# Optimization experiments

Hardware: AMD Instinct MI355X
Metric: run time of the kernel (lower is better)

## Reference

```python
import jax, jax.numpy as jnp
import numpy as np

B, T, D, H = 4, 2048, 1024, 16
HD = D // H


def setup_inputs() -> dict:
    key = jax.random.key(0)
    kq, kk, kv, k1, k2, k3, k4 = jax.random.split(key, 7)
    q = jax.random.normal(kq, (B, T, D), dtype=jnp.float32)
    k = jax.random.normal(kk, (B, T, D), dtype=jnp.float32)
    v = jax.random.normal(kv, (B, T, D), dtype=jnp.float32)
    # causal mask, broadcast over heads: [B, 1, T, T]
    mask = jnp.broadcast_to(jnp.tril(jnp.ones((T, T), dtype=bool)), (B, 1, T, T))
    s = 0.02
    Wq = jax.random.normal(k1, (D, D), dtype=jnp.float32) * s
    Wk = jax.random.normal(k2, (D, D), dtype=jnp.float32) * s
    Wv = jax.random.normal(k3, (D, D), dtype=jnp.float32) * s
    Wo = jax.random.normal(k4, (D, D), dtype=jnp.float32) * s
    return {"q": q, "k": k, "v": v, "mask": mask,
            "Wq": Wq, "Wk": Wk, "Wv": Wv, "Wo": Wo}


def reference(q, k, v, mask, Wq, Wk, Wv, Wo):
    scale = HD ** -0.5
    # nn.Linear: y = x @ W.T  (bias=False)
    qh = (q @ Wq.T).reshape(B, T, H, HD).transpose(0, 2, 1, 3)  # [B,H,T,HD]
    kh = (k @ Wk.T).reshape(B, -1, H, HD).transpose(0, 2, 1, 3)
    vh = (v @ Wv.T).reshape(B, -1, H, HD).transpose(0, 2, 1, 3)
    scores = jnp.einsum('bhqd,bhkd->bhqk', qh, kh) * scale  # [B,H,T,T]
    # dropout p=0.0 -> identity (applied pre-mask in original)
    scores = jnp.where(mask, scores, -jnp.inf)
    probs = jax.nn.softmax(scores, axis=-1)
    attn = jnp.einsum('bhqk,bhkd->bhqd', probs, vh)  # [B,H,T,HD]
    attn = attn.transpose(0, 2, 1, 3).reshape(B, T, D)
    return attn @ Wo.T
```

## Files before the change

kernel.cpp:

```cpp
#include <hip/hip_runtime.h>
#include <stdint.h>

#define B_  4
#define T_  2048
#define D_  1024
#define H_  16
#define HD_ 64
#define KK_ 1024

typedef __bf16 bf16_t;
typedef __bf16 bf16x8 __attribute__((ext_vector_type(8)));
typedef float  f32x4  __attribute__((ext_vector_type(4)));
typedef float  f32x16 __attribute__((ext_vector_type(16)));

__device__ __forceinline__ uint16_t f2bf(float f) {
  uint32_t x = __float_as_uint(f);
  uint32_t r = (x + 0x7fffu + ((x >> 16) & 1u)) >> 16;
  return (uint16_t)r;
}

__device__ __forceinline__ uint32_t pack2(float a, float b) {
  return (uint32_t)f2bf(a) | ((uint32_t)f2bf(b) << 16);
}

__device__ __forceinline__ float exp2a(float x) {
  float r;
  asm("v_exp_f32 %0, %1" : "=v"(r) : "v"(x));
  return r;
}

__device__ __forceinline__ uint32_t cvtpk(float a, float b) {
  uint32_t r;
  asm("v_cvt_pk_bf16_f32 %0, %1, %2" : "=v"(r) : "v"(a), "v"(b));
  return r;
}

__device__ __forceinline__ void plswap(uint32_t& a, uint32_t& b) {
  asm("v_permlane32_swap_b32 %0, %1" : "+v"(a), "+v"(b));
}

__device__ __forceinline__ void gll16(const void* g, void* l) {
  __builtin_amdgcn_global_load_lds(
      (const __attribute__((address_space(1))) void*)g,
      (__attribute__((address_space(3))) void*)l, 16, 0, 0);
}

__global__ __launch_bounds__(256) void cvt3(const float* __restrict__ s0,
                                            const float* __restrict__ s1,
                                            const float* __restrict__ s2,
                                            uint16_t* __restrict__ d0,
                                            uint16_t* __restrict__ d1,
                                            uint16_t* __restrict__ d2) {
  const float* in = blockIdx.y == 0 ? s0 : (blockIdx.y == 1 ? s1 : s2);
  uint16_t* out = blockIdx.y == 0 ? d0 : (blockIdx.y == 1 ? d1 : d2);
  int i = (blockIdx.x * 256 + threadIdx.x) * 8;
  float4 a = *(const float4*)(in + i);
  float4 b = *(const float4*)(in + i + 4);
  uint4 u;
  u.x = pack2(a.x, a.y);
  u.y = pack2(a.z, a.w);
  u.z = pack2(b.x, b.y);
  u.w = pack2(b.z, b.w);
  *(uint4*)(out + i) = u;
}

__global__ __launch_bounds__(256) void cvtW(const float* __restrict__ s0,
                                            const float* __restrict__ s1,
                                            const float* __restrict__ s2,
                                            const float* __restrict__ s3,
                                            uint16_t* __restrict__ d0,
                                            uint16_t* __restrict__ d1,
                                            uint16_t* __restrict__ d2,
                                            uint16_t* __restrict__ d3) {
  const float* in = blockIdx.y == 0 ? s0 : (blockIdx.y == 1 ? s1 :
                    (blockIdx.y == 2 ? s2 : s3));
  uint16_t* out = blockIdx.y == 0 ? d0 : (blockIdx.y == 1 ? d1 :
                  (blockIdx.y == 2 ? d2 : d3));
  int i = (blockIdx.x * 256 + threadIdx.x) * 8;
  float4 a = *(const float4*)(in + i);
  float4 b = *(const float4*)(in + i + 4);
  uint4 u;
  u.x = pack2(a.x, a.y);
  u.y = pack2(a.z, a.w);
  u.z = pack2(b.x, b.y);
  u.w = pack2(b.z, b.w);
  *(uint4*)(out + i) = u;
}

__global__ __launch_bounds__(512, 2)
void gemm8(const uint16_t* __restrict__ a0, const uint16_t* __restrict__ a1,
           const uint16_t* __restrict__ a2, const uint16_t* __restrict__ w0,
           const uint16_t* __restrict__ w1, const uint16_t* __restrict__ w2,
           void* __restrict__ o0, void* __restrict__ o1, void* __restrict__ o2,
           int mode_base, float scale0) {
  __shared__ __align__(16) uint16_t Ab[4][128 * 32];
  __shared__ __align__(16) uint16_t Bb[4][256 * 32];

  const int nwg = gridDim.x;
  const int bid = blockIdx.x;
  const int cpx = nwg >> 3;
  const int swz = (bid & 7) * cpx + (bid >> 3);
  const int g = swz >> 8;
  const int r = swz & 255;
  const int mt = r >> 2, nt = r & 3;
  const int m0 = mt * 128, n0 = nt * 256;

  const uint16_t* A = g == 0 ? a0 : (g == 1 ? a1 : a2);
  const uint16_t* W = g == 0 ? w0 : (g == 1 ? w1 : w2);
  void* Out = g == 0 ? o0 : (g == 1 ? o1 : o2);
  const int mode = mode_base + g;
  const float scale = (mode == 0) ? scale0 : 1.0f;

  const int tid = threadIdx.x;
  const int wid = tid >> 6, lane = tid & 63;
  const int fr = lane & 15, fq = lane >> 4;
  const int wm = wid >> 2, wn = wid & 3;

  f32x4 acc[4][4];
#pragma unroll
  for (int i = 0; i < 4; ++i)
#pragma unroll
    for (int j = 0; j < 4; ++j) acc[i][j] = (f32x4){0.f, 0.f, 0.f, 0.f};

  const int NT = KK_ / 32;

#define STAGE(bi, t)                                                          \
  do {                                                                        \
    {                                                                         \
      int row = wid * 16 + (lane >> 2);                                       \
      int ch = (lane & 3) ^ ((row >> 1) & 3);                                 \
      gll16(A + (size_t)(m0 + row) * KK_ + (t) * 32 + ch * 8,                 \
            &Ab[bi][wid * 512]);                                              \
    }                                                                         \
    _Pragma("unroll")                                                         \
    for (int c = 0; c < 2; ++c) {                                             \
      int row = c * 128 + wid * 16 + (lane >> 2);                             \
      int ch = (lane & 3) ^ ((row >> 1) & 3);                                 \
      gll16(W + (size_t)(n0 + row) * KK_ + (t) * 32 + ch * 8,                 \
            &Bb[bi][c * 4096 + wid * 512]);                                   \
    }                                                                         \
  } while (0)

  STAGE(0, 0);
  STAGE(1, 1);
  STAGE(2, 2);
  asm volatile("s_waitcnt vmcnt(6)" ::: "memory");
  __builtin_amdgcn_s_barrier();

#pragma unroll 4
  for (int t = 0; t < NT; ++t) {
    const int cur = t & 3;
    bf16x8 af[4], bfr[4];
#pragma unroll
    for (int i = 0; i < 4; ++i) {
      int ra = wm * 64 + i * 16 + fr;
      af[i] = *(const bf16x8*)&Ab[cur][ra * 32 + ((fq ^ ((ra >> 1) & 3)) << 3)];
      int rb = wn * 64 + i * 16 + fr;
      bfr[i] = *(const bf16x8*)&Bb[cur][rb * 32 + ((fq ^ ((rb >> 1) & 3)) << 3)];
    }
    if (t + 3 < NT) STAGE((t + 3) & 3, t + 3);
    __builtin_amdgcn_s_setprio(1);
#pragma unroll
    for (int mf = 0; mf < 4; ++mf)
#pragma unroll
      for (int nf = 0; nf < 4; ++nf)
        acc[mf][nf] = __builtin_amdgcn_mfma_f32_16x16x32_bf16(af[mf], bfr[nf],
                                                              acc[mf][nf], 0, 0, 0);
    __builtin_amdgcn_s_setprio(0);
    if (t + 1 < NT) {
      if (t + 3 < NT) {
        asm volatile("s_waitcnt vmcnt(6)" ::: "memory");
      } else if (t + 2 < NT) {
        asm volatile("s_waitcnt vmcnt(3)" ::: "memory");
      } else {
        asm volatile("s_waitcnt vmcnt(0)" ::: "memory");
      }
      __builtin_amdgcn_s_barrier();
    }
  }
#undef STAGE

#pragma unroll
  for (int mf = 0; mf < 4; ++mf) {
#pragma unroll
    for (int nf = 0; nf < 4; ++nf) {
      int m = m0 + wm * 64 + mf * 16 + fq * 4;
      int n = n0 + wn * 64 + nf * 16 + fr;
      if (mode == 2) {
        int b = m >> 11, t = m & (T_ - 1);
        int h = n >> 6, hd = n & 63;
        uint2 pk;
        pk.x = pack2(acc[mf][nf][0], acc[mf][nf][1]);
        pk.y = pack2(acc[mf][nf][2], acc[mf][nf][3]);
        uint16_t* dst = (uint16_t*)Out + ((((size_t)b * H_ + h) * HD_ + hd) * T_ + t);
        *(uint2*)dst = pk;
      } else if (mode == 3) {
#pragma unroll
        for (int rr = 0; rr < 4; ++rr)
          ((float*)Out)[(size_t)(m + rr) * D_ + n] = acc[mf][nf][rr];
      } else {
#pragma unroll
        for (int rr = 0; rr < 4; ++rr) {
          int mm = m + rr;
          int b = mm >> 11, t = mm & (T_ - 1);
          int h = n >> 6, hd = n & 63;
          ((uint16_t*)Out)[((((size_t)b * H_ + h) * T_ + t) << 6) + hd] =
              f2bf(acc[mf][nf][rr] * scale);
        }
      }
    }
  }
}

__global__ __launch_bounds__(512)
void attn_fwd(const uint16_t* __restrict__ Qh, const uint16_t* __restrict__ Kh,
              const uint16_t* __restrict__ Vt, uint16_t* __restrict__ O) {
  __shared__ __align__(16) uint16_t SB[4][64 * 64];

  const int tid = threadIdx.x, wid = tid >> 6, lane = tid & 63;
  const int ql = lane & 31, hi = lane >> 5;
  const int bid = blockIdx.x;
  const int qb = (T_ / 256 - 1) - (bid >> 6);
  const int bh = bid & 63;
  const int q0 = qb * 256;
  const int wq0 = q0 + wid * 32;
  const size_t hoff = (size_t)bh * T_ * HD_;
  const uint16_t* Qp = Qh + hoff;
  const uint16_t* Kp = Kh + hoff;
  const uint16_t* Vp = Vt + hoff;

  bf16x8 qf[4];
  {
    const uint16_t* qrow = Qp + (size_t)(wq0 + ql) * 64 + hi * 8;
#pragma unroll
    for (int ks = 0; ks < 4; ++ks) qf[ks] = *(const bf16x8*)(qrow + ks * 16);
  }

  float m = -1e30f, l = 0.f;
  f32x16 acc[2];
#pragma unroll
  for (int mo = 0; mo < 2; ++mo)
#pragma unroll
    for (int r = 0; r < 16; ++r) acc[mo][r] = 0.f;

  const int ntiles = 4 * qb + 4;

#define STAGE(buf, t)                                                        \
  do {                                                                       \
    int row = wid * 8 + (lane >> 3);                                         \
    int sw = ((lane & 7) ^ (row & 7)) << 3;                                  \
    gll16(Kp + (size_t)((t) * 64 + row) * 64 + sw, &SB[buf][wid * 512]);     \
    gll16(Vp + (size_t)row * T_ + (t) * 64 + sw, &SB[2 + (buf)][wid * 512]); \
  } while (0)

  STAGE(0, 0);
  asm volatile("s_waitcnt vmcnt(0)" ::: "memory");
  __builtin_amdgcn_s_barrier();

  for (int it = 0; it < ntiles; ++it) {
    const int cur = it & 1;
    if (it + 1 < ntiles) STAGE(cur ^ 1, it + 1);

    if (it * 64 <= wq0 + 31) {
      f32x16 st[2];
#pragma unroll
      for (int mm = 0; mm < 2; ++mm)
#pragma unroll
        for (int r = 0; r < 16; ++r) st[mm][r] = 0.f;
#pragma unroll
      for (int ks = 0; ks < 4; ++ks) {
#pragma unroll
        for (int mm = 0; mm < 2; ++mm) {
          int row = mm * 32 + ql;
          int ch = (ks * 2 + hi) ^ (row & 7);
          bf16x8 kf = *(const bf16x8*)&SB[cur][row * 64 + ch * 8];
          st[mm] = __builtin_amdgcn_mfma_f32_32x32x16_bf16(kf, qf[ks], st[mm], 0, 0, 0);
        }
      }

      if (it * 64 + 63 > wq0) {
        int qg = wq0 + ql;
#pragma unroll
        for (int mm = 0; mm < 2; ++mm)
#pragma unroll
          for (int r = 0; r < 16; ++r) {
            int kv = it * 64 + mm * 32 + (r & 3) + 8 * (r >> 2) + 4 * hi;
            if (kv > qg) st[mm][r] = -1e30f;
          }
      }

      float pm = st[0][0];
#pragma unroll
      for (int r = 1; r < 16; ++r) pm = fmaxf(pm, st[0][r]);
#pragma unroll
      for (int r = 0; r < 16; ++r) pm = fmaxf(pm, st[1][r]);
      pm = fmaxf(pm, __shfl_xor(pm, 32));

      if (__any(pm > m + 8.f)) {
        float mn = fmaxf(m, pm);
        float sf = exp2a(m - mn);
        m = mn;
        l *= sf;
#pragma unroll
        for (int mo = 0; mo < 2; ++mo)
#pragma unroll
          for (int r = 0; r < 16; ++r) acc[mo][r] *= sf;
      }

      float rs = 0.f;
#pragma unroll
      for (int mm = 0; mm < 2; ++mm)
#pragma unroll
        for (int r = 0; r < 16; ++r) {
          float p = exp2a(st[mm][r] - m);
          st[mm][r] = p;
          rs += p;
        }
      rs += __shfl_xor(rs, 32);
      l += rs;

      bf16x8 pf[4];
#pragma unroll
      for (int mm = 0; mm < 2; ++mm)
#pragma unroll
        for (int g = 0; g < 2; ++g) {
          uint32_t a1 = cvtpk(st[mm][8 * g + 0], st[mm][8 * g + 1]);
          uint32_t a2 = cvtpk(st[mm][8 * g + 2], st[mm][8 * g + 3]);
          uint32_t b1 = cvtpk(st[mm][8 * g + 4], st[mm][8 * g + 5]);
          uint32_t b2 = cvtpk(st[mm][8 * g + 6], st[mm][8 * g + 7]);
          plswap(a1, b1);
          plswap(a2, b2);
          union { uint32_t w[4]; bf16x8 v; } u;
          u.w[0] = a1; u.w[1] = a2; u.w[2] = b1; u.w[3] = b2;
          pf[mm * 2 + g] = u.v;
        }

#pragma unroll
      for (int ks = 0; ks < 4; ++ks) {
#pragma unroll
        for (int mo = 0; mo < 2; ++mo) {
          int row = mo * 32 + ql;
          int ch = (ks * 2 + hi) ^ (row & 7);
          bf16x8 vf = *(const bf16x8*)&SB[2 + cur][row * 64 + ch * 8];
          acc[mo] = __builtin_amdgcn_mfma_f32_32x32x16_bf16(vf, pf[ks], acc[mo], 0, 0, 0);
        }
      }
    }

    asm volatile("s_waitcnt vmcnt(0)" ::: "memory");
    __builtin_amdgcn_s_barrier();
  }
#undef STAGE

  __syncthreads();
  uint16_t* ost = &SB[0][0];
  {
    float inv = 1.0f / l;
    uint16_t* wst = ost + wid * 2048;
#pragma unroll
    for (int mo = 0; mo < 2; ++mo)
#pragma unroll
      for (int r = 0; r < 16; r += 2) {
        int hd = mo * 32 + (r & 3) + 8 * (r >> 2) + 4 * hi;
        uint32_t pk = pack2(acc[mo][r] * inv, acc[mo][r + 1] * inv);
        int col = hd ^ ((ql & 7) << 3);
        *(uint32_t*)&wst[ql * 64 + col] = pk;
      }
  }
  __syncthreads();
  {
    int row = tid >> 1, half = tid & 1;
    int r7 = row & 7;
    int b = bh >> 4, h = bh & 15;
    size_t g = (size_t)(b * T_ + q0 + row) * D_ + h * 64 + half * 32;
#pragma unroll
    for (int j = 0; j < 4; ++j) {
      int cc = half * 4 + j;
      uint4 val = *(const uint4*)&ost[row * 64 + (cc ^ r7) * 8];
      *(uint4*)&O[g + j * 8] = val;
    }
  }
}

extern "C" void kernel_launch(void* const* d_in, const int* in_sizes, int n_in,
                              void* d_out, int out_size, void* d_ws, size_t ws_size,
                              hipStream_t stream) {
  (void)in_sizes; (void)n_in; (void)out_size; (void)ws_size;
  const float* q  = (const float*)d_in[0];
  const float* k  = (const float*)d_in[1];
  const float* v  = (const float*)d_in[2];
  const float* Wq = (const float*)d_in[4];
  const float* Wk = (const float*)d_in[5];
  const float* Wv = (const float*)d_in[6];
  const float* Wo = (const float*)d_in[7];

  uint8_t* ws = (uint8_t*)d_ws;
  const size_t MB = 1u << 20;
  uint16_t* WQB = (uint16_t*)(ws + 0 * MB);
  uint16_t* WKB = (uint16_t*)(ws + 2 * MB);
  uint16_t* WVB = (uint16_t*)(ws + 4 * MB);
  uint16_t* WOB = (uint16_t*)(ws + 6 * MB);
  uint16_t* XQ  = (uint16_t*)(ws + 8 * MB);
  uint16_t* XK  = (uint16_t*)(ws + 24 * MB);
  uint16_t* XV  = (uint16_t*)(ws + 40 * MB);
  uint16_t* QH  = (uint16_t*)(ws + 56 * MB);
  uint16_t* KH  = (uint16_t*)(ws + 72 * MB);
  uint16_t* VT  = (uint16_t*)(ws + 88 * MB);
  uint16_t* AC  = (uint16_t*)(ws + 8 * MB);

  cvt3<<<dim3(B_ * T_ * D_ / 2048, 3), 256, 0, stream>>>(q, k, v, XQ, XK, XV);
  cvtW<<<dim3(D_ * D_ / 2048, 4), 256, 0, stream>>>(Wq, Wk, Wv, Wo, WQB, WKB, WVB, WOB);

  const float qscale = 0.125f * 1.44269504088896340736f;

  gemm8<<<dim3(768), 512, 0, stream>>>(XQ, XK, XV, WQB, WKB, WVB,
                                       QH, KH, VT, 0, qscale);

  attn_fwd<<<dim3(T_ / 256 * 64), 512, 0, stream>>>(QH, KH, VT, AC);

  gemm8<<<dim3(256), 512, 0, stream>>>(AC, nullptr, nullptr, WOB, nullptr, nullptr,
                                       d_out, nullptr, nullptr, 3, 1.0f);
}
```

Measured before the change: 175.7 us.

## Deepen GEMM K-tile to 64 and triple-buffer attention K/V loads

The projection GEMM moves from a 4-stage ring of 32-wide K tiles to a 3-stage ring of 64-wide K tiles. This halves the number of barrier and wait iterations and doubles the MFMA work between syncs, with a new XOR swizzle for the 64-wide rows. The attention kernel moves from double to triple buffering of K/V tiles, prefetching two tiles ahead and waiting with vmcnt(2) instead of draining all loads every iteration. Both changes use more LDS, which may lower occupancy.

```diff
diff --git a/kernel.cpp b/kernel.cpp
--- a/kernel.cpp
+++ b/kernel.cpp
@@ -93,8 +93,8 @@
            const uint16_t* __restrict__ w1, const uint16_t* __restrict__ w2,
            void* __restrict__ o0, void* __restrict__ o1, void* __restrict__ o2,
            int mode_base, float scale0) {
-  __shared__ __align__(16) uint16_t Ab[4][128 * 32];
-  __shared__ __align__(16) uint16_t Bb[4][256 * 32];
+  __shared__ __align__(16) uint16_t Ab[3][128 * 64];
+  __shared__ __align__(16) uint16_t Bb[3][256 * 64];
 
   const int nwg = gridDim.x;
   const int bid = blockIdx.x;
@@ -115,6 +115,7 @@
   const int wid = tid >> 6, lane = tid & 63;
   const int fr = lane & 15, fq = lane >> 4;
   const int wm = wid >> 2, wn = wid & 3;
+  const int srow = lane >> 3, c8 = lane & 7;
 
   f32x4 acc[4][4];
 #pragma unroll
@@ -122,61 +123,78 @@
 #pragma unroll
     for (int j = 0; j < 4; ++j) acc[i][j] = (f32x4){0.f, 0.f, 0.f, 0.f};
 
-  const int NT = KK_ / 32;
+  const int NT = KK_ / 64;
 
 #define STAGE(bi, t)                                                          \
   do {                                                                        \
-    {                                                                         \
-      int row = wid * 16 + (lane >> 2);                                       \
-      int ch = (lane & 3) ^ ((row >> 1) & 3);                                 \
-      gll16(A + (size_t)(m0 + row) * KK_ + (t) * 32 + ch * 8,                 \
-            &Ab[bi][wid * 512]);                                              \
+    _Pragma("unroll")                                                         \
+    for (int c = 0; c < 2; ++c) {                                             \
+      int row = c * 64 + wid * 8 + srow;                                      \
+      int sw = (c8 ^ (row & 7)) << 3;                                         \
+      gll16(A + (size_t)(m0 + row) * KK_ + (t) * 64 + sw,                     \
+            &Ab[bi][c * 4096 + wid * 512]);                                   \
     }                                                                         \
     _Pragma("unroll")                                                         \
-    for (int c = 0; c < 2; ++c) {                                             \
-      int row = c * 128 + wid * 16 + (lane >> 2);                             \
-      int ch = (lane & 3) ^ ((row >> 1) & 3);                                 \
-      gll16(W + (size_t)(n0 + row) * KK_ + (t) * 32 + ch * 8,                 \
+    for (int c = 0; c < 4; ++c) {                                             \
+      int row = c * 64 + wid * 8 + srow;                                      \
+      int sw = (c8 ^ (row & 7)) << 3;                                         \
+      gll16(W + (size_t)(n0 + row) * KK_ + (t) * 64 + sw,                     \
             &Bb[bi][c * 4096 + wid * 512]);                                   \
     }                                                                         \
   } while (0)
 
   STAGE(0, 0);
   STAGE(1, 1);
-  STAGE(2, 2);
   asm volatile("s_waitcnt vmcnt(6)" ::: "memory");
   __builtin_amdgcn_s_barrier();
 
-#pragma unroll 4
+  int cur = 0;
   for (int t = 0; t < NT; ++t) {
-    const int cur = t & 3;
-    bf16x8 af[4], bfr[4];
+    const uint16_t* Ac = &Ab[cur][0];
+    const uint16_t* Bc = &Bb[cur][0];
+    bf16x8 af0[4], bf0[4];
 #pragma unroll
     for (int i = 0; i < 4; ++i) {
       int ra = wm * 64 + i * 16 + fr;
-      af[i] = *(const bf16x8*)&Ab[cur][ra * 32 + ((fq ^ ((ra >> 1) & 3)) << 3)];
+      af0[i] = *(const bf16x8*)&Ac[ra * 64 + ((fq ^ (ra & 7)) << 3)];
       int rb = wn * 64 + i * 16 + fr;
-      bfr[i] = *(const bf16x8*)&Bb[cur][rb * 32 + ((fq ^ ((rb >> 1) & 3)) << 3)];
-    }
-    if (t + 3 < NT) STAGE((t + 3) & 3, t + 3);
+      bf0[i] = *(const bf16x8*)&Bc[rb * 64 + ((fq ^ (rb & 7)) << 3)];
+    }
+    if (t + 2 < NT) {
+      int nb = cur + 2; if (nb >= 3) nb -= 3;
+      STAGE(nb, t + 2);
+    }
+    bf16x8 af1[4], bf1[4];
+#pragma unroll
+    for (int i = 0; i < 4; ++i) {
+      int ra = wm * 64 + i * 16 + fr;
+      af1[i] = *(const bf16x8*)&Ac[ra * 64 + (((4 + fq) ^ (ra & 7)) << 3)];
+      int rb = wn * 64 + i * 16 + fr;
+      bf1[i] = *(const bf16x8*)&Bc[rb * 64 + (((4 + fq) ^ (rb & 7)) << 3)];
+    }
     __builtin_amdgcn_s_setprio(1);
 #pragma unroll
     for (int mf = 0; mf < 4; ++mf)
 #pragma unroll
       for (int nf = 0; nf < 4; ++nf)
-        acc[mf][nf] = __builtin_amdgcn_mfma_f32_16x16x32_bf16(af[mf], bfr[nf],
+        acc[mf][nf] = __builtin_amdgcn_mfma_f32_16x16x32_bf16(af0[mf], bf0[nf],
+                                                              acc[mf][nf], 0, 0, 0);
+#pragma unroll
+    for (int mf = 0; mf < 4; ++mf)
+#pragma unroll
+      for (int nf = 0; nf < 4; ++nf)
+        acc[mf][nf] = __builtin_amdgcn_mfma_f32_16x16x32_bf16(af1[mf], bf1[nf],
                                                               acc[mf][nf], 0, 0, 0);
     __builtin_amdgcn_s_setprio(0);
     if (t + 1 < NT) {
-      if (t + 3 < NT) {
+      if (t + 2 < NT) {
         asm volatile("s_waitcnt vmcnt(6)" ::: "memory");
-      } else if (t + 2 < NT) {
-        asm volatile("s_waitcnt vmcnt(3)" ::: "memory");
       } else {
         asm volatile("s_waitcnt vmcnt(0)" ::: "memory");
       }
       __builtin_amdgcn_s_barrier();
     }
+    ++cur; if (cur == 3) cur = 0;
   }
 #undef STAGE
 
@@ -215,7 +233,7 @@
 __global__ __launch_bounds__(512)
 void attn_fwd(const uint16_t* __restrict__ Qh, const uint16_t* __restrict__ Kh,
               const uint16_t* __restrict__ Vt, uint16_t* __restrict__ O) {
-  __shared__ __align__(16) uint16_t SB[4][64 * 64];
+  __shared__ __align__(16) uint16_t SB[6][64 * 64];
 
   const int tid = threadIdx.x, wid = tid >> 6, lane = tid & 63;
   const int ql = lane & 31, hi = lane >> 5;
@@ -250,16 +268,20 @@
     int row = wid * 8 + (lane >> 3);                                         \
     int sw = ((lane & 7) ^ (row & 7)) << 3;                                  \
     gll16(Kp + (size_t)((t) * 64 + row) * 64 + sw, &SB[buf][wid * 512]);     \
-    gll16(Vp + (size_t)row * T_ + (t) * 64 + sw, &SB[2 + (buf)][wid * 512]); \
+    gll16(Vp + (size_t)row * T_ + (t) * 64 + sw, &SB[3 + (buf)][wid * 512]); \
   } while (0)
 
   STAGE(0, 0);
-  asm volatile("s_waitcnt vmcnt(0)" ::: "memory");
+  if (ntiles > 1) STAGE(1, 1);
+  asm volatile("s_waitcnt vmcnt(2)" ::: "memory");
   __builtin_amdgcn_s_barrier();
 
+  int cur = 0;
   for (int it = 0; it < ntiles; ++it) {
-    const int cur = it & 1;
-    if (it + 1 < ntiles) STAGE(cur ^ 1, it + 1);
+    if (it + 2 < ntiles) {
+      int nb = cur + 2; if (nb >= 3) nb -= 3;
+      STAGE(nb, it + 2);
+    }
 
     if (it * 64 <= wq0 + 31) {
       f32x16 st[2];
@@ -341,14 +363,21 @@
         for (int mo = 0; mo < 2; ++mo) {
           int row = mo * 32 + ql;
           int ch = (ks * 2 + hi) ^ (row & 7);
-          bf16x8 vf = *(const bf16x8*)&SB[2 + cur][row * 64 + ch * 8];
+          bf16x8 vf = *(const bf16x8*)&SB[3 + cur][row * 64 + ch * 8];
           acc[mo] = __builtin_amdgcn_mfma_f32_32x32x16_bf16(vf, pf[ks], acc[mo], 0, 0, 0);
         }
       }
     }
 
-    asm volatile("s_waitcnt vmcnt(0)" ::: "memory");
-    __builtin_amdgcn_s_barrier();
+    if (it + 1 < ntiles) {
+      if (it + 2 < ntiles) {
+        asm volatile("s_waitcnt vmcnt(2)" ::: "memory");
+      } else {
+        asm volatile("s_waitcnt vmcnt(0)" ::: "memory");
+      }
+      __builtin_amdgcn_s_barrier();
+    }
+    ++cur; if (cur == 3) cur = 0;
   }
 #undef STAGE
 
```

Result: faster. 164.0 us (-6.7%).
